# Kernel tuning notes

Hardware: AMD Instinct MI355X
Metric: run time of the kernel (lower is better)

## Reference

```python
import jax, jax.numpy as jnp
import numpy as np

FEATURE_DIM = 256
NUM_COEDGES = 200000


def setup_inputs() -> dict:
    key = jax.random.key(0)
    ks = jax.random.split(key, 13)
    d = FEATURE_DIM
    n = NUM_COEDGES
    scale = 1.0 / np.sqrt(d)
    inp = {
        "features": jax.random.normal(ks[0], (n, d), dtype=jnp.float32),
        "next_indices": jax.random.randint(ks[1], (n,), 0, n),
        "prev_indices": jax.random.randint(ks[2], (n,), 0, n),
        "mate_indices": jax.random.randint(ks[3], (n,), 0, n),
        # Linear params (torch Linear: y = x @ W.T + b); store as [d, d] for x @ W
        "W_self": jax.random.uniform(ks[4], (d, d), jnp.float32, -scale, scale),
        "b_self": jax.random.uniform(ks[5], (d,), jnp.float32, -scale, scale),
        "W_next": jax.random.uniform(ks[6], (d, d), jnp.float32, -scale, scale),
        "b_next": jax.random.uniform(ks[7], (d,), jnp.float32, -scale, scale),
        "W_prev": jax.random.uniform(ks[8], (d, d), jnp.float32, -scale, scale),
        "b_prev": jax.random.uniform(ks[9], (d,), jnp.float32, -scale, scale),
        "W_mate": jax.random.uniform(ks[10], (d, d), jnp.float32, -scale, scale),
        "b_mate": jax.random.uniform(ks[11], (d,), jnp.float32, -scale, scale),
    }
    return inp


def reference(features, next_indices, prev_indices, mate_indices,
              W_self, b_self, W_next, b_next, W_prev, b_prev, W_mate, b_mate):
    h = features  # [n, d]
    h_self = h @ W_self + b_self
    h_next = h[next_indices] @ W_next + b_next
    h_prev = h[prev_indices] @ W_prev + b_prev
    h_mate = h[mate_indices] @ W_mate + b_mate
    return jax.nn.relu(h_self + h_next + h_prev + h_mate)
```

## Files before the change

kernel.cpp:

```cpp
#include <hip/hip_runtime.h>
#include <stdint.h>


#define D 256
#define BM 64

typedef __bf16 bf16x8 __attribute__((ext_vector_type(8)));
typedef float f32x4 __attribute__((ext_vector_type(4)));

static __device__ __forceinline__ uint16_t f32_to_bf16_rne(uint32_t u) {
    return (uint16_t)((u + 0x7FFFu + ((u >> 16) & 1u)) >> 16);
}

__global__ void k_conv(const float* __restrict__ f, uint16_t* __restrict__ o, long total) {
    long i = ((long)blockIdx.x * blockDim.x + threadIdx.x) * 8;
    if (i + 8 > total) return;
    const uint32_t* p = (const uint32_t*)(f + i);
    uint32_t v[8];
    *(uint4*)(v)     = *(const uint4*)(p);
    *(uint4*)(v + 4) = *(const uint4*)(p + 4);
    union { uint16_t u16[8]; uint4 v4; } r;
#pragma unroll
    for (int j = 0; j < 8; j++) r.u16[j] = f32_to_bf16_rne(v[j]);
    *(uint4*)(o + i) = r.v4;
}

__global__ void k_pack(const float* __restrict__ Ws, const float* __restrict__ Wn,
                       const float* __restrict__ Wp, const float* __restrict__ Wm,
                       uint16_t* __restrict__ Bp) {
    int b = blockIdx.x;
    int l = threadIdx.x;
    int ksg = b >> 4, nt = b & 15;
    int ph = ksg >> 3;
    const float* W = (ph == 0) ? Ws : (ph == 1) ? Wn : (ph == 2) ? Wp : Wm;
    int kl = (ksg & 7) * 32 + (l >> 4) * 8;
    int n  = nt * 16 + (l & 15);
    uint16_t* dst = Bp + ((size_t)b * 64 + l) * 8;
#pragma unroll
    for (int j = 0; j < 8; j++) {
        uint32_t u = __builtin_bit_cast(uint32_t, W[(size_t)(kl + j) * D + n]);
        dst[j] = f32_to_bf16_rne(u);
    }
}

__global__ void k_bias(const float* __restrict__ b0, const float* __restrict__ b1,
                       const float* __restrict__ b2, const float* __restrict__ b3,
                       float* __restrict__ btot) {
    int t = threadIdx.x;
    if (t < D) btot[t] = b0[t] + b1[t] + b2[t] + b3[t];
}

typedef __attribute__((address_space(1))) uint32_t gu32;
typedef __attribute__((address_space(3))) uint32_t lu32;

__global__ __launch_bounds__(256) void k_gemm(
    const uint16_t* __restrict__ fb,
    const int* __restrict__ ni, const int* __restrict__ pi, const int* __restrict__ mi,
    const uint16_t* __restrict__ Bp, const float* __restrict__ btot,
    float* __restrict__ out, int nrows)
{
    __shared__ uint16_t As[BM * D];
    const int t  = threadIdx.x;
    const int w  = t >> 6;
    const int l  = t & 63;
    const int ml = l & 15;
    const int q  = l >> 4;
    const int m0 = blockIdx.x * BM;

    f32x4 acc[4][4] = {};

    const int rpar = w * 16 + (l >> 5);
    const int cs   = l & 31;

    for (int p = 0; p < 4; p++) {
        const int* idx = (p == 0) ? (const int*)0 : (p == 1) ? ni : (p == 2) ? pi : mi;
        __syncthreads();
#pragma unroll
        for (int e = 0; e < 8; e++) {
            int r    = rpar + e * 2;
            int rowg = m0 + r;
            if (rowg >= nrows) rowg = nrows - 1;
            int gr = idx ? idx[rowg] : rowg;
            int cc = cs ^ (r & 7);
            const uint16_t* g = fb + (size_t)gr * D + cc * 8;
            uint16_t* s = &As[(w * 16 + e * 2) * D];
            __builtin_amdgcn_global_load_lds((gu32*)g, (lu32*)s, 16, 0, 0);
        }
        __syncthreads();

        const uint16_t* bbase = Bp + (((size_t)p * 128 + w * 4) * 64 + l) * 8;
#pragma unroll 2
        for (int ks = 0; ks < 8; ks++) {
            bf16x8 bfr[4];
#pragma unroll
            for (int j = 0; j < 4; j++)
                bfr[j] = *(const bf16x8*)(bbase + ((size_t)ks * 16 + j) * 64 * 8);
            bf16x8 afr[4];
#pragma unroll
            for (int mt = 0; mt < 4; mt++) {
                int r  = mt * 16 + ml;
                int ch = (ks * 4 + q) ^ (r & 7);
                afr[mt] = *(const bf16x8*)&As[r * D + ch * 8];
            }
#pragma unroll
            for (int mt = 0; mt < 4; mt++)
#pragma unroll
                for (int j = 0; j < 4; j++)
                    acc[mt][j] = __builtin_amdgcn_mfma_f32_16x16x32_bf16(
                        afr[mt], bfr[j], acc[mt][j], 0, 0, 0);
        }
    }

#pragma unroll
    for (int j = 0; j < 4; j++) {
        int n = (w * 4 + j) * 16 + ml;
        float bv = btot[n];
#pragma unroll
        for (int mt = 0; mt < 4; mt++) {
#pragma unroll
            for (int rg = 0; rg < 4; rg++) {
                int row = m0 + mt * 16 + q * 4 + rg;
                if (row < nrows) {
                    float v = acc[mt][j][rg] + bv;
                    out[(size_t)row * D + n] = v > 0.f ? v : 0.f;
                }
            }
        }
    }
}

__global__ void k_naive(const float* __restrict__ f,
                        const int* __restrict__ ni, const int* __restrict__ pi,
                        const int* __restrict__ mi,
                        const float* __restrict__ Ws, const float* __restrict__ bs,
                        const float* __restrict__ Wn, const float* __restrict__ bn,
                        const float* __restrict__ Wp, const float* __restrict__ bp,
                        const float* __restrict__ Wm, const float* __restrict__ bm,
                        float* __restrict__ out) {
    int row = blockIdx.x, n = threadIdx.x;
    const float* f0 = f + (size_t)row * D;
    const float* f1 = f + (size_t)ni[row] * D;
    const float* f2 = f + (size_t)pi[row] * D;
    const float* f3 = f + (size_t)mi[row] * D;
    float s = bs[n] + bn[n] + bp[n] + bm[n];
    for (int k = 0; k < D; k++)
        s += f0[k] * Ws[k * D + n] + f1[k] * Wn[k * D + n] +
             f2[k] * Wp[k * D + n] + f3[k] * Wm[k * D + n];
    out[(size_t)row * D + n] = s > 0.f ? s : 0.f;
}

extern "C" void kernel_launch(void* const* d_in, const int* in_sizes, int n_in,
                              void* d_out, int out_size, void* d_ws, size_t ws_size,
                              hipStream_t stream) {
    const float* feat = (const float*)d_in[0];
    const int*   ni   = (const int*)d_in[1];
    const int*   pi   = (const int*)d_in[2];
    const int*   mi   = (const int*)d_in[3];
    const float* Ws   = (const float*)d_in[4];
    const float* bs   = (const float*)d_in[5];
    const float* Wn   = (const float*)d_in[6];
    const float* bn   = (const float*)d_in[7];
    const float* Wp   = (const float*)d_in[8];
    const float* bp   = (const float*)d_in[9];
    const float* Wm   = (const float*)d_in[10];
    const float* bm   = (const float*)d_in[11];
    float* out = (float*)d_out;

    int nrows = in_sizes[1];
    size_t feat_elems = (size_t)nrows * D;
    size_t fb_bytes   = feat_elems * 2;
    size_t bp_off     = fb_bytes;
    size_t bias_off   = bp_off + (size_t)1024 * D * 2;
    size_t need       = bias_off + (size_t)D * 4;

    if (ws_size < need) {
        k_naive<<<nrows, D, 0, stream>>>(feat, ni, pi, mi, Ws, bs, Wn, bn, Wp, bp, Wm, bm, out);
        return;
    }

    uint16_t* fbuf = (uint16_t*)d_ws;
    uint16_t* Bpk  = (uint16_t*)((char*)d_ws + bp_off);
    float*    btot = (float*)((char*)d_ws + bias_off);

    long total = (long)feat_elems;
    int cblocks = (int)((total / 8 + 255) / 256);
    k_conv<<<cblocks, 256, 0, stream>>>(feat, fbuf, total);
    k_pack<<<512, 64, 0, stream>>>(Ws, Wn, Wp, Wm, Bpk);
    k_bias<<<1, 256, 0, stream>>>(bs, bn, bp, bm, btot);
    k_gemm<<<(nrows + BM - 1) / BM, 256, 0, stream>>>(fbuf, ni, pi, mi, Bpk, btot, out, nrows);
}
```

Before: 567.6 us.

## Double-buffer gathered A tiles across phases and precompute gather offsets

```diff
diff --git a/kernel.cpp b/kernel.cpp
--- a/kernel.cpp
+++ b/kernel.cpp
@@ -13,16 +13,19 @@
 }
 
 __global__ void k_conv(const float* __restrict__ f, uint16_t* __restrict__ o, long total) {
-    long i = ((long)blockIdx.x * blockDim.x + threadIdx.x) * 8;
-    if (i + 8 > total) return;
-    const uint32_t* p = (const uint32_t*)(f + i);
-    uint32_t v[8];
-    *(uint4*)(v)     = *(const uint4*)(p);
-    *(uint4*)(v + 4) = *(const uint4*)(p + 4);
-    union { uint16_t u16[8]; uint4 v4; } r;
-#pragma unroll
-    for (int j = 0; j < 8; j++) r.u16[j] = f32_to_bf16_rne(v[j]);
-    *(uint4*)(o + i) = r.v4;
+    long base = (long)blockIdx.x * 2048;
+    int t = threadIdx.x;
+#pragma unroll
+    for (int pass = 0; pass < 2; pass++) {
+        long i = base + pass * 1024 + (long)t * 4;
+        if (i + 4 > total) return;
+        uint32_t v[4];
+        *(uint4*)v = *(const uint4*)(f + i);
+        union { uint16_t u16[4]; uint2 v2; } r;
+#pragma unroll
+        for (int j = 0; j < 4; j++) r.u16[j] = f32_to_bf16_rne(v[j]);
+        *(uint2*)(o + i) = r.v2;
+    }
 }
 
 __global__ void k_pack(const float* __restrict__ Ws, const float* __restrict__ Wn,
@@ -53,13 +56,13 @@
 typedef __attribute__((address_space(1))) uint32_t gu32;
 typedef __attribute__((address_space(3))) uint32_t lu32;
 
-__global__ __launch_bounds__(256) void k_gemm(
+__global__ __launch_bounds__(256, 2) void k_gemm(
     const uint16_t* __restrict__ fb,
     const int* __restrict__ ni, const int* __restrict__ pi, const int* __restrict__ mi,
     const uint16_t* __restrict__ Bp, const float* __restrict__ btot,
     float* __restrict__ out, int nrows)
 {
-    __shared__ uint16_t As[BM * D];
+    __shared__ uint16_t As[2][BM * D];
     const int t  = threadIdx.x;
     const int w  = t >> 6;
     const int l  = t & 63;
@@ -72,44 +75,97 @@
     const int rpar = w * 16 + (l >> 5);
     const int cs   = l & 31;
 
-    for (int p = 0; p < 4; p++) {
-        const int* idx = (p == 0) ? (const int*)0 : (p == 1) ? ni : (p == 2) ? pi : mi;
-        __syncthreads();
-#pragma unroll
-        for (int e = 0; e < 8; e++) {
-            int r    = rpar + e * 2;
-            int rowg = m0 + r;
-            if (rowg >= nrows) rowg = nrows - 1;
-            int gr = idx ? idx[rowg] : rowg;
-            int cc = cs ^ (r & 7);
-            const uint16_t* g = fb + (size_t)gr * D + cc * 8;
-            uint16_t* s = &As[(w * 16 + e * 2) * D];
-            __builtin_amdgcn_global_load_lds((gu32*)g, (lu32*)s, 16, 0, 0);
-        }
-        __syncthreads();
-
-        const uint16_t* bbase = Bp + (((size_t)p * 128 + w * 4) * 64 + l) * 8;
-#pragma unroll 2
-        for (int ks = 0; ks < 8; ks++) {
-            bf16x8 bfr[4];
-#pragma unroll
-            for (int j = 0; j < 4; j++)
-                bfr[j] = *(const bf16x8*)(bbase + ((size_t)ks * 16 + j) * 64 * 8);
-            bf16x8 afr[4];
-#pragma unroll
-            for (int mt = 0; mt < 4; mt++) {
-                int r  = mt * 16 + ml;
-                int ch = (ks * 4 + q) ^ (r & 7);
-                afr[mt] = *(const bf16x8*)&As[r * D + ch * 8];
-            }
-#pragma unroll
-            for (int mt = 0; mt < 4; mt++)
-#pragma unroll
-                for (int j = 0; j < 4; j++)
-                    acc[mt][j] = __builtin_amdgcn_mfma_f32_16x16x32_bf16(
-                        afr[mt], bfr[j], acc[mt][j], 0, 0, 0);
-        }
-    }
+    uint32_t off0[8], off1[8], off2[8], off3[8];
+#pragma unroll
+    for (int e = 0; e < 8; e++) {
+        int r = rpar + e * 2;
+        int rowg = m0 + r; if (rowg >= nrows) rowg = nrows - 1;
+        uint32_t co = (uint32_t)((cs ^ (r & 7)) * 16);
+        off0[e] = (uint32_t)rowg * (D * 2) + co;
+        off1[e] = (uint32_t)ni[rowg] * (D * 2) + co;
+        off2[e] = (uint32_t)pi[rowg] * (D * 2) + co;
+        off3[e] = (uint32_t)mi[rowg] * (D * 2) + co;
+    }
+
+#define STAGE(OFFA, BUF) do { \
+        uint16_t* _s = &As[BUF][(w * 16) * D]; \
+        _Pragma("unroll") \
+        for (int e = 0; e < 8; e++) { \
+            const char* _g = (const char*)fb + (OFFA)[e]; \
+            __builtin_amdgcn_global_load_lds((const gu32*)_g, (lu32*)(_s + e * 2 * D), 16, 0, 0); \
+        } \
+    } while (0)
+
+#define KSTEP(BUF, BB, KS) do { \
+        bf16x8 bfr[4]; \
+        _Pragma("unroll") \
+        for (int j = 0; j < 4; j++) bfr[j] = *(const bf16x8*)((BB) + ((KS) * 16 + j) * 512); \
+        bf16x8 afr[4]; \
+        _Pragma("unroll") \
+        for (int mt = 0; mt < 4; mt++) { \
+            int r = mt * 16 + ml; \
+            int ch = ((KS) * 4 + q) ^ (r & 7); \
+            afr[mt] = *(const bf16x8*)&As[BUF][r * D + ch * 8]; \
+        } \
+        _Pragma("unroll") \
+        for (int mt = 0; mt < 4; mt++) \
+            _Pragma("unroll") \
+            for (int j = 0; j < 4; j++) \
+                acc[mt][j] = __builtin_amdgcn_mfma_f32_16x16x32_bf16(afr[mt], bfr[j], acc[mt][j], 0, 0, 0); \
+    } while (0)
+
+#define KSTEP_PRE(BUF, BPRE, KS) do { \
+        bf16x8 afr[4]; \
+        _Pragma("unroll") \
+        for (int mt = 0; mt < 4; mt++) { \
+            int r = mt * 16 + ml; \
+            int ch = ((KS) * 4 + q) ^ (r & 7); \
+            afr[mt] = *(const bf16x8*)&As[BUF][r * D + ch * 8]; \
+        } \
+        _Pragma("unroll") \
+        for (int mt = 0; mt < 4; mt++) \
+            _Pragma("unroll") \
+            for (int j = 0; j < 4; j++) \
+                acc[mt][j] = __builtin_amdgcn_mfma_f32_16x16x32_bf16(afr[mt], (BPRE)[j], acc[mt][j], 0, 0, 0); \
+    } while (0)
+
+#define WAITBAR() do { \
+        asm volatile("s_waitcnt vmcnt(0)" ::: "memory"); \
+        __builtin_amdgcn_s_barrier(); \
+        __builtin_amdgcn_sched_barrier(0); \
+    } while (0)
+
+#define PHASE(P, BUF, OFFNEXT, LAST) do { \
+        WAITBAR(); \
+        const uint16_t* bb = Bp + (((size_t)(P) * 128 + w * 4) * 64 + l) * 8; \
+        KSTEP(BUF, bb, 0); KSTEP(BUF, bb, 1); KSTEP(BUF, bb, 2); \
+        KSTEP(BUF, bb, 3); KSTEP(BUF, bb, 4); KSTEP(BUF, bb, 5); \
+        bf16x8 b6[4], b7[4]; \
+        _Pragma("unroll") \
+        for (int j = 0; j < 4; j++) { \
+            b6[j] = *(const bf16x8*)(bb + (6 * 16 + j) * 512); \
+            b7[j] = *(const bf16x8*)(bb + (7 * 16 + j) * 512); \
+        } \
+        if (!(LAST)) { \
+            __builtin_amdgcn_sched_barrier(0); \
+            STAGE(OFFNEXT, (BUF) ^ 1); \
+            __builtin_amdgcn_sched_barrier(0); \
+        } \
+        KSTEP_PRE(BUF, b6, 6); \
+        KSTEP_PRE(BUF, b7, 7); \
+    } while (0)
+
+    STAGE(off0, 0);
+    PHASE(0, 0, off1, 0);
+    PHASE(1, 1, off2, 0);
+    PHASE(2, 0, off3, 0);
+    PHASE(3, 1, off0, 1);
+
+#undef PHASE
+#undef WAITBAR
+#undef KSTEP_PRE
+#undef KSTEP
+#undef STAGE
 
 #pragma unroll
     for (int j = 0; j < 4; j++) {
@@ -183,7 +239,7 @@
     float*    btot = (float*)((char*)d_ws + bias_off);
 
     long total = (long)feat_elems;
-    int cblocks = (int)((total / 8 + 255) / 256);
+    int cblocks = (int)((total + 2047) / 2048);
     k_conv<<<cblocks, 256, 0, stream>>>(feat, fbuf, total);
     k_pack<<<512, 64, 0, stream>>>(Ws, Wn, Wp, Wm, Bpk);
     k_bias<<<1, 256, 0, stream>>>(bs, bn, bp, bm, btot);
```

Result: faster. 537.6 us (-5.3%).
